# Kernel tuning notes

Hardware: AMD Instinct MI355X
Metric: run time of the kernel (lower is better)

Reference implementation:

```python
import jax, jax.numpy as jnp
import numpy as np

B, S, D, H, DH = 2, 2048, 1024, 16, 64
R_ATTN, R_OUT, I, R_FC1, R_FC2 = 32, 512, 4096, 512, 512
LN_EPS = 1e-5


def _layernorm(x, g, b):
    mu = jnp.mean(x, axis=-1, keepdims=True)
    var = jnp.mean(jnp.square(x - mu), axis=-1, keepdims=True)
    return (x - mu) * jax.lax.rsqrt(var + LN_EPS) * g + b


def setup_inputs() -> dict:
    key = jax.random.key(0)
    ks = jax.random.split(key, 16)
    std = 0.02
    return {
        'hidden_states': jax.random.normal(ks[0], (B, S, D), jnp.float32),
        'ln1_g': jnp.ones((D,), jnp.float32),
        'ln1_b': jnp.zeros((D,), jnp.float32),
        'ln2_g': jnp.ones((D,), jnp.float32),
        'ln2_b': jnp.zeros((D,), jnp.float32),
        'q_U': jax.random.normal(ks[1], (D, H, R_ATTN), jnp.float32) * std,
        'q_V': jax.random.normal(ks[2], (H, R_ATTN, DH), jnp.float32) * std,
        'q_b': jnp.zeros((H, DH), jnp.float32),
        'k_U': jax.random.normal(ks[3], (D, H, R_ATTN), jnp.float32) * std,
        'k_V': jax.random.normal(ks[4], (H, R_ATTN, DH), jnp.float32) * std,
        'k_b': jnp.zeros((H, DH), jnp.float32),
        'v_U': jax.random.normal(ks[5], (D, H, R_ATTN), jnp.float32) * std,
        'v_V': jax.random.normal(ks[6], (H, R_ATTN, DH), jnp.float32) * std,
        'v_b': jnp.zeros((H, DH), jnp.float32),
        'out_U': jax.random.normal(ks[7], (D, R_OUT), jnp.float32) * std,
        'out_V': jax.random.normal(ks[8], (R_OUT, D), jnp.float32) * std,
        'out_b': jnp.zeros((D,), jnp.float32),
        'fc1_U': jax.random.normal(ks[9], (D, R_FC1), jnp.float32) * std,
        'fc1_V': jax.random.normal(ks[10], (R_FC1, I), jnp.float32) * std,
        'fc1_b': jnp.zeros((I,), jnp.float32),
        'fc2_U': jax.random.normal(ks[11], (I, R_FC2), jnp.float32) * std,
        'fc2_V': jax.random.normal(ks[12], (R_FC2, D), jnp.float32) * std,
        'fc2_b': jnp.zeros((D,), jnp.float32),
    }


def reference(hidden_states, ln1_g, ln1_b, ln2_g, ln2_b,
              q_U, q_V, q_b, k_U, k_V, k_b, v_U, v_V, v_b,
              out_U, out_V, out_b, fc1_U, fc1_V, fc1_b, fc2_U, fc2_V, fc2_b):
    Bx, Sx, Dx = hidden_states.shape
    scale = 1.0 / np.sqrt(DH).astype(np.float32)
    x = _layernorm(hidden_states, ln1_g, ln1_b)
    # low-rank per-head QKV: [B,S,D]x[D,H,r]x[H,r,dh] -> [B,H,S,dh]
    Q = jnp.einsum('bsd,dhr,hre->bhse', x, q_U, q_V) + q_b[None, :, None, :]
    K = jnp.einsum('bsd,dhr,hre->bhse', x, k_U, k_V) + k_b[None, :, None, :]
    V = jnp.einsum('bsd,dhr,hre->bhse', x, v_U, v_V) + v_b[None, :, None, :]
    scores = jnp.einsum('bhse,bhte->bhst', Q, K) * scale  # [B,H,S,S]
    causal = jnp.tril(jnp.ones((Sx, Sx), bool))
    neg_inf = jnp.finfo(scores.dtype).min
    scores = jnp.where(causal, scores, neg_inf)
    probs = jax.nn.softmax(scores, axis=-1)
    Y = jnp.einsum('bhst,bhte->bhse', probs, V)
    Y = Y.transpose(0, 2, 1, 3).reshape(Bx, Sx, Dx)  # merge heads
    Y = (Y @ out_U) @ out_V + out_b
    h = hidden_states + Y
    z = _layernorm(h, ln2_g, ln2_b)
    h1 = jax.nn.gelu((z @ fc1_U) @ fc1_V + fc1_b, approximate=False)
    h2 = (h1 @ fc2_U) @ fc2_V + fc2_b
    return h + h2
```

## Files before the change

### kernel.cpp

```cpp
#include <hip/hip_runtime.h>
#include <cstdint>
#include <cstddef>


#define NTOK 4096
#define DM   1024
#define SEQ  2048

typedef __attribute__((ext_vector_type(8))) __bf16 bf16x8;
typedef __attribute__((ext_vector_type(4))) __bf16 bf16x4;
typedef __attribute__((ext_vector_type(4))) float  f32x4;

__device__ __forceinline__ f32x4 mfma16(bf16x8 a, bf16x8 b, f32x4 c) {
  return __builtin_amdgcn_mfma_f32_16x16x32_bf16(a, b, c, 0, 0, 0);
}

__device__ __forceinline__ void gload16(const __bf16* g, __bf16* l) {
  __builtin_amdgcn_global_load_lds(
      (const __attribute__((address_space(1))) void*)g,
      (__attribute__((address_space(3))) void*)l, 16, 0, 0);
}

__global__ __launch_bounds__(256) void transpose_k(const float* __restrict__ in,
                                                   __bf16* __restrict__ out,
                                                   int R, int C) {
  __shared__ __bf16 t[32][33];
  int tx = threadIdx.x & 31, ty = threadIdx.x >> 5;
  int r0 = blockIdx.y * 32, c0 = blockIdx.x * 32;
#pragma unroll
  for (int i = 0; i < 32; i += 8)
    t[ty + i][tx] = (__bf16)in[(size_t)(r0 + ty + i) * C + c0 + tx];
  __syncthreads();
#pragma unroll
  for (int i = 0; i < 32; i += 8)
    out[(size_t)(c0 + ty + i) * R + r0 + tx] = t[tx][ty + i];
}

__global__ __launch_bounds__(256) void prep_k(
    const float* __restrict__ qb, const float* __restrict__ kb,
    const float* __restrict__ vb, float* __restrict__ bqkv,
    const float* __restrict__ outU, __bf16* __restrict__ outUT,
    const float* __restrict__ outV, __bf16* __restrict__ outVT,
    const float* __restrict__ f1U,  __bf16* __restrict__ f1UT,
    const float* __restrict__ f1V,  __bf16* __restrict__ f1VT,
    const float* __restrict__ f2V,  __bf16* __restrict__ f2VT,
    const float* __restrict__ f2U,  __bf16* __restrict__ f2UT) {
  int blk = blockIdx.x;
  if (blk < 12) {
    int i = blk * 256 + threadIdx.x;
    bqkv[i] = (i < 1024) ? qb[i] : (i < 2048 ? kb[i - 1024] : vb[i - 2048]);
    return;
  }
  int t = blk - 12;
  const float* in; __bf16* out; int R, C;
  if (t < 512)       { in = outU; out = outUT; R = 1024; C = 512;  }
  else if (t < 1024) { in = outV; out = outVT; R = 512;  C = 1024; t -= 512; }
  else if (t < 1536) { in = f1U;  out = f1UT;  R = 1024; C = 512;  t -= 1024; }
  else if (t < 3584) { in = f1V;  out = f1VT;  R = 512;  C = 4096; t -= 1536; }
  else if (t < 4096) { in = f2V;  out = f2VT;  R = 512;  C = 1024; t -= 3584; }
  else               { in = f2U;  out = f2UT;  R = 4096; C = 512;  t -= 4096; }
  int ct = C >> 5;
  int c0 = (t % ct) * 32, r0 = (t / ct) * 32;
  __shared__ __bf16 tt[32][33];
  int tx = threadIdx.x & 31, ty = threadIdx.x >> 5;
#pragma unroll
  for (int i = 0; i < 32; i += 8)
    tt[ty + i][tx] = (__bf16)in[(size_t)(r0 + ty + i) * C + c0 + tx];
  __syncthreads();
#pragma unroll
  for (int i = 0; i < 32; i += 8)
    out[(size_t)(c0 + ty + i) * R + r0 + tx] = tt[tx][ty + i];
}

__global__ __launch_bounds__(256) void trans_v(const __bf16* __restrict__ qkv,
                                               __bf16* __restrict__ VT) {
  __shared__ __bf16 t[32][33];
  int tx = threadIdx.x & 31, ty = threadIdx.x >> 5;
  int bh = blockIdx.z, b = bh >> 4, h = bh & 15;
  int k0 = blockIdx.x * 32, d0 = blockIdx.y * 32;
#pragma unroll
  for (int i = 0; i < 32; i += 8)
    t[ty + i][tx] = qkv[(size_t)(b * SEQ + k0 + ty + i) * 3072 + 2048 + h * 64 + d0 + tx];
  __syncthreads();
#pragma unroll
  for (int i = 0; i < 32; i += 8)
    VT[(size_t)(bh * 64 + d0 + ty + i) * SEQ + k0 + tx] = t[tx][ty + i];
}

__global__ __launch_bounds__(256) void combine_uv(const float* __restrict__ qU,
                                                  const float* __restrict__ qV,
                                                  const float* __restrict__ kU,
                                                  const float* __restrict__ kV,
                                                  const float* __restrict__ vU,
                                                  const float* __restrict__ vV,
                                                  __bf16* __restrict__ WT) {
  __shared__ float sV[2048];
  int tid = threadIdx.x;
  int blk = blockIdx.x;
  int sel = blk >> 7;
  int rem = blk & 127;
  int h = rem >> 3, dc = rem & 7;
  int d0 = dc << 7;
  const float* U = sel == 0 ? qU : (sel == 1 ? kU : vU);
  const float* V = sel == 0 ? qV : (sel == 1 ? kV : vV);
  for (int i = tid; i < 2048; i += 256) sV[i] = V[h * 2048 + i];
  int d = d0 + (tid & 127);
  int eh = tid >> 7;
  const float* up = U + (size_t)d * 512 + h * 32;
  float u[32];
#pragma unroll
  for (int i = 0; i < 8; i++)
    *(float4*)&u[i * 4] = *(const float4*)(up + i * 4);
  __syncthreads();
  int e0 = eh * 32;
#pragma unroll
  for (int eg = 0; eg < 8; eg++) {
    float ax = 0.f, ay = 0.f, az = 0.f, aw = 0.f;
#pragma unroll
    for (int r = 0; r < 32; r++) {
      float4 v4 = *(const float4*)&sV[r * 64 + e0 + eg * 4];
      ax += u[r] * v4.x; ay += u[r] * v4.y;
      az += u[r] * v4.z; aw += u[r] * v4.w;
    }
    size_t prow = (size_t)(sel * 1024 + h * 64 + e0 + eg * 4) * 1024 + d;
    WT[prow]        = (__bf16)ax;
    WT[prow + 1024] = (__bf16)ay;
    WT[prow + 2048] = (__bf16)az;
    WT[prow + 3072] = (__bf16)aw;
  }
}

__global__ __launch_bounds__(256) void cast_k(const float* __restrict__ in,
                                              __bf16* __restrict__ out, int n) {
  int i = blockIdx.x * 256 + threadIdx.x;
  if (i < n) out[i] = (__bf16)in[i];
}

__global__ __launch_bounds__(256) void merge4_k(const float* __restrict__ p,
                                                __bf16* __restrict__ out) {
  int i = blockIdx.x * 256 + threadIdx.x;
  float s = (p[i] + p[i + 2097152]) + (p[i + 4194304] + p[i + 6291456]);
  out[i] = (__bf16)s;
}

template <int TWO>
__global__ __launch_bounds__(256) void ln_k(const float* __restrict__ x,
                                            const __bf16* __restrict__ x2,
                                            const float* __restrict__ g,
                                            const float* __restrict__ b,
                                            __bf16* __restrict__ out) {
  int row = blockIdx.x, tid = threadIdx.x;
  const float* xr = x + (size_t)row * DM;
  float v[4], s = 0.f, ss = 0.f;
#pragma unroll
  for (int i = 0; i < 4; i++) {
    int c = i * 256 + tid;
    v[i] = xr[c];
    if (TWO) v[i] += (float)x2[(size_t)row * DM + c];
    s += v[i]; ss += v[i] * v[i];
  }
#pragma unroll
  for (int m = 1; m < 64; m <<= 1) { s += __shfl_xor(s, m); ss += __shfl_xor(ss, m); }
  __shared__ float rs_[4], rss[4];
  if ((tid & 63) == 0) { rs_[tid >> 6] = s; rss[tid >> 6] = ss; }
  __syncthreads();
  s  = rs_[0] + rs_[1] + rs_[2] + rs_[3];
  ss = rss[0] + rss[1] + rss[2] + rss[3];
  float mu  = s * (1.f / 1024.f);
  float var = ss * (1.f / 1024.f) - mu * mu;
  float rstd = rsqrtf(var + 1e-5f);
#pragma unroll
  for (int i = 0; i < 4; i++) {
    int c = i * 256 + tid;
    out[(size_t)row * DM + c] = (__bf16)((v[i] - mu) * rstd * g[c] + b[c]);
  }
}

template <int EPI, int BN>
__global__ __launch_bounds__(256) void gemm_bt(const __bf16* __restrict__ A,
                                               const __bf16* __restrict__ BT,
                                               void* __restrict__ Cv,
                                               const float* __restrict__ bias,
                                               const float* __restrict__ resF,
                                               const __bf16* __restrict__ resB,
                                               int M, int N, int K) {
  constexpr int WR = (BN == 128) ? 4 : 2;
  __shared__ alignas(16) __bf16 la[2][128 * 32];
  __shared__ alignas(16) __bf16 lb[2][BN * 32];
  int tid = threadIdx.x;
  int lane = tid & 63;
  int wave = tid >> 6;
  int quad = lane >> 4, l15 = lane & 15;
  int gx = gridDim.x;
  int nwg = gx * gridDim.y;
  int flat = blockIdx.y * gx + blockIdx.x;
  if ((nwg & 7) == 0) flat = (flat & 7) * (nwg >> 3) + (flat >> 3);
  int bm = (flat / gx) * 128, bn = (flat % gx) * BN;
  int wm = (BN == 128) ? (wave >> 1) * 64 : wave * 32;
  int wn = (BN == 128) ? (wave & 1) * 64 : 0;
  int lr = lane >> 2;
  int lc = (((lane & 3) ^ ((lr >> 1) & 3))) * 8;
  const __bf16* ga = A  + (size_t)(bm + wave * 32 + lr) * K + lc;
  const __bf16* gb = BT + (size_t)(bn + wave * (BN == 128 ? 32 : 16) + lr) * K + lc;
  int ksw = ((l15 >> 1) & 3) * 8;
  f32x4 acc[WR][4] = {};

  auto stage = [&](int k0, int b) {
    __bf16* lab = &la[b][wave * 1024];
    gload16(ga + k0, lab);
    gload16(ga + (size_t)16 * K + k0, lab + 512);
    if (BN == 128) {
      __bf16* lbb = &lb[b][wave * 1024];
      gload16(gb + k0, lbb);
      gload16(gb + (size_t)16 * K + k0, lbb + 512);
    } else {
      gload16(gb + k0, &lb[b][wave * 512]);
    }
  };

  stage(0, 0);
  __syncthreads();
  for (int k0 = 0; k0 < K; k0 += 32) {
    int b = (k0 >> 5) & 1;
    if (k0 + 32 < K) stage(k0 + 32, b ^ 1);
    bf16x8 af[WR], bfr[4];
#pragma unroll
    for (int i = 0; i < WR; i++)
      af[i] = *(const bf16x8*)&la[b][(wm + i * 16 + l15) * 32 + (quad * 8 ^ ksw)];
#pragma unroll
    for (int j = 0; j < 4; j++)
      bfr[j] = *(const bf16x8*)&lb[b][(wn + j * 16 + l15) * 32 + (quad * 8 ^ ksw)];
#pragma unroll
    for (int i = 0; i < WR; i++)
#pragma unroll
      for (int j = 0; j < 4; j++)
        acc[i][j] = mfma16(af[i], bfr[j], acc[i][j]);
    __syncthreads();
  }
#pragma unroll
  for (int i = 0; i < WR; i++) {
#pragma unroll
    for (int j = 0; j < 4; j++) {
      int col = bn + wn + j * 16 + l15;
      float bv = bias ? bias[col] : 0.f;
#pragma unroll
      for (int r = 0; r < 4; r++) {
        int row = bm + wm + i * 16 + quad * 4 + r;
        size_t idx = (size_t)row * N + col;
        float v = acc[i][j][r] + bv;
        if (EPI == 0) {
          ((__bf16*)Cv)[idx] = (__bf16)v;
        } else if (EPI == 1) {
          float y = 0.79788456080286536f * fmaf(0.044715f * v, v * v, v);
          float u = exp2f(y * 2.885390081777926f);
          float th = (u - 1.f) / (u + 1.f);
          v = 0.5f * v * (1.f + th);
          ((__bf16*)Cv)[idx] = (__bf16)v;
        } else {
          v += resF[idx] + (float)resB[idx];
          ((float*)Cv)[idx] = v;
        }
      }
    }
  }
}

__global__ __launch_bounds__(256) void gemm_bt64s(const __bf16* __restrict__ A,
                                                  const __bf16* __restrict__ BT,
                                                  __bf16* __restrict__ C,
                                                  int M, int N, int K) {
  __shared__ alignas(16) __bf16 la[2][64 * 32];
  __shared__ alignas(16) __bf16 lb[2][64 * 32];
  int tid = threadIdx.x;
  int lane = tid & 63;
  int wave = tid >> 6;
  int quad = lane >> 4, l15 = lane & 15;
  int gx = gridDim.x;
  int nwg = gx * gridDim.y;
  int flat = blockIdx.y * gx + blockIdx.x;
  if ((nwg & 7) == 0) flat = (flat & 7) * (nwg >> 3) + (flat >> 3);
  int bm = (flat / gx) * 64, bn = (flat % gx) * 64;
  int lr = tid >> 2;
  int lc = (((tid & 3) ^ ((lr >> 1) & 3))) * 8;
  const __bf16* ga = A  + (size_t)(bm + lr) * K + lc;
  const __bf16* gb = BT + (size_t)(bn + lr) * K + lc;
  int ksw = ((l15 >> 1) & 3) * 8;
  f32x4 acc[4] = {};

  auto stage = [&](int k0, int b) {
    gload16(ga + k0, &la[b][tid * 8]);
    gload16(gb + k0, &lb[b][tid * 8]);
  };

  stage(0, 0);
  __syncthreads();
  for (int k0 = 0; k0 < K; k0 += 32) {
    int b = (k0 >> 5) & 1;
    if (k0 + 32 < K) stage(k0 + 32, b ^ 1);
    bf16x8 af = *(const bf16x8*)&la[b][(wave * 16 + l15) * 32 + (quad * 8 ^ ksw)];
    bf16x8 bfr[4];
#pragma unroll
    for (int j = 0; j < 4; j++)
      bfr[j] = *(const bf16x8*)&lb[b][(j * 16 + l15) * 32 + (quad * 8 ^ ksw)];
#pragma unroll
    for (int j = 0; j < 4; j++)
      acc[j] = mfma16(af, bfr[j], acc[j]);
    __syncthreads();
  }
#pragma unroll
  for (int j = 0; j < 4; j++) {
    int col = bn + j * 16 + l15;
#pragma unroll
    for (int r = 0; r < 4; r++) {
      int row = bm + wave * 16 + quad * 4 + r;
      C[(size_t)row * N + col] = (__bf16)acc[j][r];
    }
  }
}

template <int ATOMIC>
__global__ __launch_bounds__(256) void gemm_sk(const __bf16* __restrict__ A,
                                               const __bf16* __restrict__ BT,
                                               float* __restrict__ Cf,
                                               int M, int N, int K, int KS) {
  __shared__ alignas(16) __bf16 la[2][128 * 32];
  __shared__ alignas(16) __bf16 lb[2][128 * 32];
  int tid = threadIdx.x;
  int lane = tid & 63;
  int wave = tid >> 6;
  int quad = lane >> 4, l15 = lane & 15;
  int bm = blockIdx.y * 128, bn = blockIdx.x * 128;
  int wm = (wave >> 1) * 64, wn = (wave & 1) * 64;
  int klen = K / KS;
  int kbeg = blockIdx.z * klen, kend = kbeg + klen;
  int lr = lane >> 2;
  int lc = (((lane & 3) ^ ((lr >> 1) & 3))) * 8;
  const __bf16* ga = A  + (size_t)(bm + wave * 32 + lr) * K + lc;
  const __bf16* gb = BT + (size_t)(bn + wave * 32 + lr) * K + lc;
  int ksw = ((l15 >> 1) & 3) * 8;
  f32x4 acc[4][4] = {};

  auto stage = [&](int k0, int b) {
    __bf16* lab = &la[b][wave * 1024];
    __bf16* lbb = &lb[b][wave * 1024];
    gload16(ga + k0, lab);
    gload16(ga + (size_t)16 * K + k0, lab + 512);
    gload16(gb + k0, lbb);
    gload16(gb + (size_t)16 * K + k0, lbb + 512);
  };

  stage(kbeg, 0);
  __syncthreads();
  for (int k0 = kbeg; k0 < kend; k0 += 32) {
    int b = ((k0 - kbeg) >> 5) & 1;
    if (k0 + 32 < kend) stage(k0 + 32, b ^ 1);
    bf16x8 af[4], bfr[4];
#pragma unroll
    for (int i = 0; i < 4; i++)
      af[i] = *(const bf16x8*)&la[b][(wm + i * 16 + l15) * 32 + (quad * 8 ^ ksw)];
#pragma unroll
    for (int j = 0; j < 4; j++)
      bfr[j] = *(const bf16x8*)&lb[b][(wn + j * 16 + l15) * 32 + (quad * 8 ^ ksw)];
#pragma unroll
    for (int i = 0; i < 4; i++)
#pragma unroll
      for (int j = 0; j < 4; j++)
        acc[i][j] = mfma16(af[i], bfr[j], acc[i][j]);
    __syncthreads();
  }
  float* out = ATOMIC ? Cf : Cf + (size_t)blockIdx.z * M * N;
#pragma unroll
  for (int i = 0; i < 4; i++)
#pragma unroll
    for (int j = 0; j < 4; j++) {
      int col = bn + wn + j * 16 + l15;
#pragma unroll
      for (int r = 0; r < 4; r++) {
        int row = bm + wm + i * 16 + quad * 4 + r;
        if (ATOMIC) atomicAdd(&out[(size_t)row * N + col], acc[i][j][r]);
        else        out[(size_t)row * N + col] = acc[i][j][r];
      }
    }
}

#define JOB(q, a, b) ((uint32_t)(q) | ((uint32_t)(a) << 8) | ((uint32_t)(b) << 16))
__device__ const uint32_t JOBTAB[24] = {
  JOB(7, 0, 16),  JOB(15, 0, 16), JOB(15, 16, 32),
  JOB(14, 0, 15), JOB(14, 15, 30),
  JOB(6, 0, 14),  JOB(13, 0, 14), JOB(13, 14, 28),
  JOB(12, 0, 13), JOB(12, 13, 26),
  JOB(5, 0, 12),  JOB(11, 0, 12), JOB(11, 12, 24),
  JOB(10, 0, 11), JOB(10, 11, 22),
  JOB(4, 0, 10),  JOB(9, 0, 10),  JOB(9, 10, 20),
  JOB(8, 0, 9),   JOB(8, 9, 18),
  JOB(3, 0, 8),   JOB(2, 0, 6),   JOB(1, 0, 4),   JOB(0, 0, 2),
};

__global__ __launch_bounds__(512, 6) void attn_k(const __bf16* __restrict__ QKV,
                                                 const __bf16* __restrict__ VT,
                                                 __bf16* __restrict__ Y,
                                                 float* __restrict__ Opart,
                                                 float* __restrict__ lpart) {
  const float SC = 0.18033688011112042f;
  const float C2 = 23.083120654223414f;
  __shared__ alignas(16) __bf16 lk[2][64 * 64];
  __shared__ alignas(16) __bf16 lv[2][64 * 64];
  __shared__ alignas(16) __bf16 P[8][16 * 72];
  int tid = threadIdx.x;
  int wave = tid >> 6, lane = tid & 63;
  int quad = lane >> 4, l15 = lane & 15;
  int bh = blockIdx.x & 31;
  int job = blockIdx.x >> 5;
  uint32_t jt = JOBTAB[job];
  int qb = jt & 255, kbeg = (jt >> 8) & 255, kend = (jt >> 16) & 255;
  bool split = qb >= 8;
  int b = bh >> 4, h = bh & 15;
  int q0w = (qb << 7) + wave * 16;
  const size_t RS = 3 * DM;
  const __bf16* base = QKV + (size_t)b * SEQ * RS;
  const __bf16* vtb  = VT + (size_t)bh * 64 * SEQ;

  const __bf16* qp = base + (size_t)(q0w + l15) * RS + h * 64 + quad * 8;
  bf16x8 aq0 = *(const bf16x8*)qp;
  bf16x8 aq1 = *(const bf16x8*)(qp + 32);

  int srow = tid >> 3, schunk = tid & 7;
  int sswz = (schunk ^ (srow & 7)) << 3;
  const __bf16* gk_src = base + (size_t)srow * RS + DM + h * 64 + sswz;
  const __bf16* gv_src = vtb + (size_t)srow * SEQ + sswz;

  int c0 = (quad ^ (l15 & 7)) << 3;
  int c1 = ((quad + 4) ^ (l15 & 7)) << 3;

  f32x4 zero4 = {0.f, 0.f, 0.f, 0.f};
  f32x4 O[4] = {zero4, zero4, zero4, zero4};
  float l_i = 0.f;

  int ntiles = kend - kbeg;

  gload16(gk_src + ((size_t)kbeg << 6) * RS, &lk[0][tid * 8]);
  gload16(gv_src + ((size_t)kbeg << 6),      &lv[0][tid * 8]);
  __syncthreads();

  for (int t = 0; t < ntiles; t++) {
    int kt = kbeg + t;
    int cur = t & 1;
    if (t + 1 < ntiles) {
      size_t kn = (size_t)(kt + 1) << 6;
      gload16(gk_src + kn * RS, &lk[cur ^ 1][tid * 8]);
      gload16(gv_src + kn,      &lv[cur ^ 1][tid * 8]);
    }
    int k0 = kt << 6;
    if (k0 <= q0w + 15) {
      f32x4 s[4] = {zero4, zero4, zero4, zero4};
#pragma unroll
      for (int gk = 0; gk < 4; gk++) {
        const __bf16* kr = &lk[cur][(gk * 16 + l15) * 64];
        bf16x8 kb0 = *(const bf16x8*)(kr + c0);
        bf16x8 kb1 = *(const bf16x8*)(kr + c1);
        s[gk] = mfma16(kb0, aq0, s[gk]);
        s[gk] = mfma16(kb1, aq1, s[gk]);
      }
      if (k0 + 63 <= q0w) {
#pragma unroll
        for (int gk = 0; gk < 4; gk++) {
          float p0 = exp2f(fmaf(s[gk][0], SC, -C2));
          float p1 = exp2f(fmaf(s[gk][1], SC, -C2));
          float p2 = exp2f(fmaf(s[gk][2], SC, -C2));
          float p3 = exp2f(fmaf(s[gk][3], SC, -C2));
          l_i += (p0 + p1) + (p2 + p3);
          bf16x4 pw = {(__bf16)p0, (__bf16)p1, (__bf16)p2, (__bf16)p3};
          *(bf16x4*)&P[wave][l15 * 72 + gk * 16 + quad * 4] = pw;
        }
      } else {
        int qrow = q0w + l15;
#pragma unroll
        for (int gk = 0; gk < 4; gk++) {
          int kb = k0 + gk * 16 + quad * 4;
          float p0 = (kb     <= qrow) ? exp2f(fmaf(s[gk][0], SC, -C2)) : 0.f;
          float p1 = (kb + 1 <= qrow) ? exp2f(fmaf(s[gk][1], SC, -C2)) : 0.f;
          float p2 = (kb + 2 <= qrow) ? exp2f(fmaf(s[gk][2], SC, -C2)) : 0.f;
          float p3 = (kb + 3 <= qrow) ? exp2f(fmaf(s[gk][3], SC, -C2)) : 0.f;
          l_i += (p0 + p1) + (p2 + p3);
          bf16x4 pw = {(__bf16)p0, (__bf16)p1, (__bf16)p2, (__bf16)p3};
          *(bf16x4*)&P[wave][l15 * 72 + gk * 16 + quad * 4] = pw;
        }
      }
      bf16x8 ap0 = *(const bf16x8*)&P[wave][l15 * 72 + quad * 8];
      bf16x8 ap1 = *(const bf16x8*)&P[wave][l15 * 72 + 32 + quad * 8];
#pragma unroll
      for (int nt = 0; nt < 4; nt++) {
        const __bf16* vr = &lv[cur][(nt * 16 + l15) * 64];
        bf16x8 bv0 = *(const bf16x8*)(vr + c0);
        bf16x8 bv1 = *(const bf16x8*)(vr + c1);
        O[nt] = mfma16(ap0, bv0, O[nt]);
        O[nt] = mfma16(ap1, bv1, O[nt]);
      }
    }
    __syncthreads();
  }

  l_i += __shfl_xor(l_i, 16);
  l_i += __shfl_xor(l_i, 32);
  if (!split) {
#pragma unroll
    for (int r = 0; r < 4; r++) {
      float inv = 1.f / __shfl(l_i, quad * 4 + r);
      size_t orow = (size_t)(b * SEQ + q0w + quad * 4 + r);
      __bf16* yp = Y + orow * DM + h * 64 + l15;
      yp[0]  = (__bf16)(O[0][r] * inv);
      yp[16] = (__bf16)(O[1][r] * inv);
      yp[32] = (__bf16)(O[2][r] * inv);
      yp[48] = (__bf16)(O[3][r] * inv);
    }
  } else {
#pragma unroll
    for (int r = 0; r < 4; r++) {
      int row = (q0w - 1024) + quad * 4 + r;
      float* op = Opart + (((size_t)bh << 10) + row) * 64 + l15;
      atomicAdd(op +  0, O[0][r]);
      atomicAdd(op + 16, O[1][r]);
      atomicAdd(op + 32, O[2][r]);
      atomicAdd(op + 48, O[3][r]);
    }
    if (quad == 0)
      atomicAdd(&lpart[((size_t)bh << 10) + (q0w - 1024) + l15], l_i);
  }
}

__global__ __launch_bounds__(256) void norm_k(const float* __restrict__ Op,
                                              const float* __restrict__ lp,
                                              __bf16* __restrict__ Y) {
  int idx = blockIdx.x * 256 + threadIdx.x;
  int dh = idx & 63;
  int row = (idx >> 6) & 1023;
  int bh = idx >> 16;
  int b = bh >> 4, h = bh & 15;
  float inv = 1.f / lp[(bh << 10) + row];
  Y[(size_t)(b * SEQ + 1024 + row) * DM + h * 64 + dh] = (__bf16)(Op[idx] * inv);
}

extern "C" void kernel_launch(void* const* d_in, const int* in_sizes, int n_in,
                              void* d_out, int out_size, void* d_ws, size_t ws_size,
                              hipStream_t stream) {
  (void)in_sizes; (void)n_in; (void)out_size;
  const float* hidden = (const float*)d_in[0];
  const float* ln1_g  = (const float*)d_in[1];
  const float* ln1_b  = (const float*)d_in[2];
  const float* ln2_g  = (const float*)d_in[3];
  const float* ln2_b  = (const float*)d_in[4];
  const float* q_U = (const float*)d_in[5];
  const float* q_V = (const float*)d_in[6];
  const float* q_b = (const float*)d_in[7];
  const float* k_U = (const float*)d_in[8];
  const float* k_V = (const float*)d_in[9];
  const float* k_b = (const float*)d_in[10];
  const float* v_U = (const float*)d_in[11];
  const float* v_V = (const float*)d_in[12];
  const float* v_b = (const float*)d_in[13];
  const float* out_U = (const float*)d_in[14];
  const float* out_V = (const float*)d_in[15];
  const float* out_b = (const float*)d_in[16];
  const float* fc1_U = (const float*)d_in[17];
  const float* fc1_V = (const float*)d_in[18];
  const float* fc1_b = (const float*)d_in[19];
  const float* fc2_U = (const float*)d_in[20];
  const float* fc2_V = (const float*)d_in[21];
  const float* fc2_b = (const float*)d_in[22];

  const size_t MB = 1u << 20;
  char* ws = (char*)d_ws;
  bool big = ws_size >= 112 * MB;
  __bf16* outUT = (__bf16*)(ws + 0 * MB);
  __bf16* outVT = (__bf16*)(ws + 1 * MB);
  __bf16* f1UT  = (__bf16*)(ws + 2 * MB);
  __bf16* f1VT  = (__bf16*)(ws + 3 * MB);
  __bf16* f2VT  = (__bf16*)(ws + 7 * MB);
  float*  bqkv  = (float*) (ws + 8 * MB);
  __bf16* wqkvT = (__bf16*)(ws + 9 * MB);
  __bf16* f2UT  = big ? (__bf16*)(ws + 55 * MB)
                      : (__bf16*)(ws + 9 * MB);
  __bf16* xln   = (__bf16*)(ws + 15 * MB);
  __bf16* yattn = (__bf16*)(ws + 15 * MB);
  __bf16* zbuf  = (__bf16*)(ws + 15 * MB);
  float*  t3f32 = (float*) (ws + 15 * MB);
  __bf16* t3bf  = (__bf16*)(ws + 19 * MB);
  __bf16* qkv   = (__bf16*)(ws + 23 * MB);
  __bf16* h1c   = big ? (__bf16*)(ws + 64 * MB)
                      : (__bf16*)(ws + 23 * MB);
  float*  t3p   = (float*) (ws + 96 * MB);
  __bf16* tbuf  = (__bf16*)(ws + 43 * MB);
  __bf16* VT    = (__bf16*)(ws + 47 * MB);
  __bf16* hres  = (__bf16*)(ws + 47 * MB);
  float* Opart = (float*)d_out;
  float* lpart = (float*)d_out + 2097152;

  prep_k<<<big ? 6156 : 4108, 256, 0, stream>>>(
      q_b, k_b, v_b, bqkv, out_U, outUT, out_V, outVT,
      fc1_U, f1UT, fc1_V, f1VT, fc2_V, f2VT, fc2_U, f2UT);
  combine_uv<<<384, 256, 0, stream>>>(q_U, q_V, k_U, k_V, v_U, v_V, wqkvT);

  ln_k<0><<<NTOK, 256, 0, stream>>>(hidden, nullptr, ln1_g, ln1_b, xln);
  gemm_bt<0, 128><<<dim3(24, 32), 256, 0, stream>>>(xln, wqkvT, qkv, bqkv,
                                                    nullptr, nullptr, NTOK, 3072, 1024);
  if (!big)
    transpose_k<<<dim3(16, 128), 256, 0, stream>>>(fc2_U, f2UT, 4096, 512);
  trans_v<<<dim3(64, 2, 32), 256, 0, stream>>>(qkv, VT);
  hipMemsetAsync(d_out, 0, (size_t)8519680, stream);
  attn_k<<<768, 512, 0, stream>>>(qkv, VT, yattn, Opart, lpart);
  norm_k<<<8192, 256, 0, stream>>>(Opart, lpart, yattn);
  gemm_bt64s<<<dim3(8, 64), 256, 0, stream>>>(yattn, outUT, tbuf, NTOK, 512, 1024);
  gemm_bt<0, 64><<<dim3(16, 32), 256, 0, stream>>>(tbuf, outVT, hres, out_b,
                                                   nullptr, nullptr, NTOK, 1024, 512);
  ln_k<1><<<NTOK, 256, 0, stream>>>(hidden, hres, ln2_g, ln2_b, zbuf);
  gemm_bt64s<<<dim3(8, 64), 256, 0, stream>>>(zbuf, f1UT, tbuf, NTOK, 512, 1024);
  if (big) {
    gemm_bt<1, 128><<<dim3(32, 32), 256, 0, stream>>>(tbuf, f1VT, h1c, fc1_b,
                                                      nullptr, nullptr, NTOK, 4096, 512);
    gemm_sk<0><<<dim3(4, 32, 4), 256, 0, stream>>>(h1c, f2UT, t3p,
                                                   NTOK, 512, 4096, 4);
    merge4_k<<<8192, 256, 0, stream>>>(t3p, t3bf);
  } else {
    for (int mc = 0; mc < 2; mc++) {
      __bf16* tchunk = tbuf + (size_t)mc * 2048 * 512;
      gemm_bt<1, 128><<<dim3(32, 16), 256, 0, stream>>>(tchunk, f1VT, h1c, fc1_b,
                                                        nullptr, nullptr, 2048, 4096, 512);
      hipMemsetAsync(t3f32, 0, (size_t)2048 * 512 * 4, stream);
      gemm_sk<1><<<dim3(4, 16, 4), 256, 0, stream>>>(h1c, f2UT, t3f32,
                                                     2048, 512, 4096, 4);
      cast_k<<<4096, 256, 0, stream>>>(t3f32, t3bf + (size_t)mc * 2048 * 512,
                                       2048 * 512);
    }
  }
  gemm_bt<3, 64><<<dim3(16, 32), 256, 0, stream>>>(t3bf, f2VT, (float*)d_out, fc2_b,
                                                   hidden, hres, NTOK, 1024, 512);
}
```

Baseline: 369.0 us.

## Precombine out_U·out_V into one weight and remap GEMM tiles per XCD

When the workspace is large, the out-projection factors are multiplied once into a dense 1024x1024 bf16 weight, so the attention output goes through one GEMM instead of two chained low-rank GEMMs. This drops a launch and the intermediate round-trip, at the cost of more FLOPs (K=1024 full rank versus two rank-512 products) and an extra bf16 rounding of the combined weight. A new xcd_map helper also assigns each XCD a 2D block of output tiles so that tiles sharing A rows and B columns land on the same XCD's L2. The 'big' workspace threshold rises to 128MB to make room for the new buffers.

Result: slower. 376.5 us (+2.1%).

```diff
diff --git a/kernel.cpp b/kernel.cpp
--- a/kernel.cpp
+++ b/kernel.cpp
@@ -19,6 +19,26 @@
   __builtin_amdgcn_global_load_lds(
       (const __attribute__((address_space(1))) void*)g,
       (__attribute__((address_space(3))) void*)l, 16, 0, 0);
+}
+
+__device__ __forceinline__ void xcd_map(int flat, int gx, int gy,
+                                        int BM, int BN, int& bm, int& bn) {
+  int nwg = gx * gy;
+  if ((nwg & 7) == 0) {
+    int cpx = nwg >> 3;
+    int xcd = flat & 7;
+    int loc = flat >> 3;
+    int w = cpx >> 4;
+    if ((gy & 15) == 0 && (cpx & 15) == 0 && w > 0 && gx % w == 0) {
+      int rcols = gx / w;
+      bm = ((xcd / rcols) * 16 + loc / w) * BM;
+      bn = ((xcd % rcols) * w + loc % w) * BN;
+      return;
+    }
+    flat = xcd * cpx + loc;
+  }
+  bm = (flat / gx) * BM;
+  bn = (flat % gx) * BN;
 }
 
 __global__ __launch_bounds__(256) void transpose_k(const float* __restrict__ in,
@@ -44,7 +64,8 @@
     const float* __restrict__ f1U,  __bf16* __restrict__ f1UT,
     const float* __restrict__ f1V,  __bf16* __restrict__ f1VT,
     const float* __restrict__ f2V,  __bf16* __restrict__ f2VT,
-    const float* __restrict__ f2U,  __bf16* __restrict__ f2UT) {
+    const float* __restrict__ f2U,  __bf16* __restrict__ f2UT,
+    __bf16* __restrict__ outUc) {
   int blk = blockIdx.x;
   if (blk < 12) {
     int i = blk * 256 + threadIdx.x;
@@ -52,6 +73,15 @@
     return;
   }
   int t = blk - 12;
+  if (t >= 6144) {
+    int i = (t - 6144) * 2048 + threadIdx.x * 8;
+    float4 a = *(const float4*)(outU + i);
+    float4 b = *(const float4*)(outU + i + 4);
+    bf16x8 o = {(__bf16)a.x, (__bf16)a.y, (__bf16)a.z, (__bf16)a.w,
+                (__bf16)b.x, (__bf16)b.y, (__bf16)b.z, (__bf16)b.w};
+    *(bf16x8*)(outUc + i) = o;
+    return;
+  }
   const float* in; __bf16* out; int R, C;
   if (t < 512)       { in = outU; out = outUT; R = 1024; C = 512;  }
   else if (t < 1024) { in = outV; out = outVT; R = 512;  C = 1024; t -= 512; }
@@ -191,11 +221,9 @@
   int lane = tid & 63;
   int wave = tid >> 6;
   int quad = lane >> 4, l15 = lane & 15;
-  int gx = gridDim.x;
-  int nwg = gx * gridDim.y;
-  int flat = blockIdx.y * gx + blockIdx.x;
-  if ((nwg & 7) == 0) flat = (flat & 7) * (nwg >> 3) + (flat >> 3);
-  int bm = (flat / gx) * 128, bn = (flat % gx) * BN;
+  int flat = blockIdx.y * gridDim.x + blockIdx.x;
+  int bm, bn;
+  xcd_map(flat, gridDim.x, gridDim.y, 128, BN, bm, bn);
   int wm = (BN == 128) ? (wave >> 1) * 64 : wave * 32;
   int wn = (BN == 128) ? (wave & 1) * 64 : 0;
   int lr = lane >> 2;
@@ -275,11 +303,9 @@
   int lane = tid & 63;
   int wave = tid >> 6;
   int quad = lane >> 4, l15 = lane & 15;
-  int gx = gridDim.x;
-  int nwg = gx * gridDim.y;
-  int flat = blockIdx.y * gx + blockIdx.x;
-  if ((nwg & 7) == 0) flat = (flat & 7) * (nwg >> 3) + (flat >> 3);
-  int bm = (flat / gx) * 64, bn = (flat % gx) * 64;
+  int flat = blockIdx.y * gridDim.x + blockIdx.x;
+  int bm, bn;
+  xcd_map(flat, gridDim.x, gridDim.y, 64, 64, bm, bn);
   int lr = tid >> 2;
   int lc = (((tid & 3) ^ ((lr >> 1) & 3))) * 8;
   const __bf16* ga = A  + (size_t)(bm + lr) * K + lc;
@@ -329,7 +355,9 @@
   int lane = tid & 63;
   int wave = tid >> 6;
   int quad = lane >> 4, l15 = lane & 15;
-  int bm = blockIdx.y * 128, bn = blockIdx.x * 128;
+  int flat = blockIdx.y * gridDim.x + blockIdx.x;
+  int bm, bn;
+  xcd_map(flat, gridDim.x, gridDim.y, 128, 128, bm, bn);
   int wm = (wave >> 1) * 64, wn = (wave & 1) * 64;
   int klen = K / KS;
   int kbeg = blockIdx.z * klen, kend = kbeg + klen;
@@ -570,7 +598,7 @@
 
   const size_t MB = 1u << 20;
   char* ws = (char*)d_ws;
-  bool big = ws_size >= 112 * MB;
+  bool big = ws_size >= 128 * MB;
   __bf16* outUT = (__bf16*)(ws + 0 * MB);
   __bf16* outVT = (__bf16*)(ws + 1 * MB);
   __bf16* f1UT  = (__bf16*)(ws + 2 * MB);
@@ -592,13 +620,19 @@
   __bf16* tbuf  = (__bf16*)(ws + 43 * MB);
   __bf16* VT    = (__bf16*)(ws + 47 * MB);
   __bf16* hres  = (__bf16*)(ws + 47 * MB);
+  __bf16* WoutT = (__bf16*)(ws + 59 * MB);
+  __bf16* outUc = (__bf16*)(ws + 61 * MB);
   float* Opart = (float*)d_out;
   float* lpart = (float*)d_out + 2097152;
 
-  prep_k<<<big ? 6156 : 4108, 256, 0, stream>>>(
+  prep_k<<<big ? 6412 : 4108, 256, 0, stream>>>(
       q_b, k_b, v_b, bqkv, out_U, outUT, out_V, outVT,
-      fc1_U, f1UT, fc1_V, f1VT, fc2_V, f2VT, fc2_U, f2UT);
+      fc1_U, f1UT, fc1_V, f1VT, fc2_V, f2VT, fc2_U, f2UT, outUc);
   combine_uv<<<384, 256, 0, stream>>>(q_U, q_V, k_U, k_V, v_U, v_V, wqkvT);
+  if (big)
+    gemm_bt<0, 64><<<dim3(16, 8), 256, 0, stream>>>(outVT, outUc, WoutT,
+                                                    nullptr, nullptr, nullptr,
+                                                    1024, 1024, 512);
 
   ln_k<0><<<NTOK, 256, 0, stream>>>(hidden, nullptr, ln1_g, ln1_b, xln);
   gemm_bt<0, 128><<<dim3(24, 32), 256, 0, stream>>>(xln, wqkvT, qkv, bqkv,
@@ -609,9 +643,14 @@
   hipMemsetAsync(d_out, 0, (size_t)8519680, stream);
   attn_k<<<768, 512, 0, stream>>>(qkv, VT, yattn, Opart, lpart);
   norm_k<<<8192, 256, 0, stream>>>(Opart, lpart, yattn);
-  gemm_bt64s<<<dim3(8, 64), 256, 0, stream>>>(yattn, outUT, tbuf, NTOK, 512, 1024);
-  gemm_bt<0, 64><<<dim3(16, 32), 256, 0, stream>>>(tbuf, outVT, hres, out_b,
-                                                   nullptr, nullptr, NTOK, 1024, 512);
+  if (big) {
+    gemm_bt<0, 64><<<dim3(16, 32), 256, 0, stream>>>(yattn, WoutT, hres, out_b,
+                                                     nullptr, nullptr, NTOK, 1024, 1024);
+  } else {
+    gemm_bt64s<<<dim3(8, 64), 256, 0, stream>>>(yattn, outUT, tbuf, NTOK, 512, 1024);
+    gemm_bt<0, 64><<<dim3(16, 32), 256, 0, stream>>>(tbuf, outVT, hres, out_b,
+                                                     nullptr, nullptr, NTOK, 1024, 512);
+  }
   ln_k<1><<<NTOK, 256, 0, stream>>>(hidden, hres, ln2_g, ln2_b, zbuf);
   gemm_bt64s<<<dim3(8, 64), 256, 0, stream>>>(zbuf, f1UT, tbuf, NTOK, 512, 1024);
   if (big) {
```
